# Kernel optimization log

Measured on AMD Instinct MI355X. Metric: run time of the kernel, lower is better.

The kernel has to match this reference:

```python
import jax, jax.numpy as jnp
import numpy as np

N, E = 100000, 1600000
IN_DIM, OUT_DIM, EDGE_DIM, HEADS = 128, 64, 16, 4
HEAD_DIM = OUT_DIM // HEADS


def setup_inputs() -> dict:
    key = jax.random.key(0)
    ks = jax.random.split(key, 8)
    x = jax.random.normal(ks[0], (N, IN_DIM), dtype=jnp.float32)
    ei = jax.random.randint(ks[1], (2, E), 0, N, dtype=jnp.int32)
    ea = jax.random.normal(ks[2], (E, EDGE_DIM), dtype=jnp.float32)
    # parameters (xavier-ish scaling)
    W_node = jax.random.normal(ks[3], (OUT_DIM, IN_DIM), dtype=jnp.float32) * (1.0 / np.sqrt(IN_DIM))
    W_edge = jax.random.normal(ks[4], (HEADS, EDGE_DIM), dtype=jnp.float32) * (1.0 / np.sqrt(EDGE_DIM))
    att_src = jax.random.normal(ks[5], (1, HEADS, HEAD_DIM), dtype=jnp.float32) * (1.0 / np.sqrt(HEAD_DIM))
    att_dst = jax.random.normal(ks[6], (1, HEADS, HEAD_DIM), dtype=jnp.float32) * (1.0 / np.sqrt(HEAD_DIM))
    bias = jnp.zeros((OUT_DIM,), dtype=jnp.float32)
    return {"x": x, "ei": ei, "ea": ea, "W_node": W_node, "W_edge": W_edge,
            "att_src": att_src, "att_dst": att_dst, "bias": bias}


def reference(x, ei, ea, W_node, W_edge, att_src, att_dst, bias):
    n = x.shape[0]
    Wh = (x @ W_node.T).reshape(n, HEADS, HEAD_DIM)          # [N,H,D]
    s, d = ei[0], ei[1]
    # per-node attention scalars, gathered per edge (avoids gathering Wh[d])
    a_src = jnp.sum(Wh * att_src, axis=-1)                    # [N,H]
    a_dst = jnp.sum(Wh * att_dst, axis=-1)                    # [N,H]
    e = jax.nn.leaky_relu(a_src[s] + a_dst[d] + ea @ W_edge.T, negative_slope=0.2)  # [E,H]
    ex = jnp.exp(e - jnp.max(e))                              # global max, as in torch e.max()
    den = jax.ops.segment_sum(ex, d, num_segments=n)          # [N,H]
    alpha = ex / (den[d] + 1e-9)                              # [E,H]
    msg = Wh[s] * alpha[:, :, None]                           # [E,H,D]
    out = jax.ops.segment_sum(msg, d, num_segments=n)         # [N,H,D]
    return jax.nn.elu(out.reshape(n, OUT_DIM) + bias)
```

## Files before the change

kernel.cpp:

```cpp
#include <hip/hip_runtime.h>
#include <math.h>

#define NN 100000
#define NE 1600000
#define IND 128
#define OUTD 64
#define ED 16
#define NH 4
#define HD 16
#define NB1 98

typedef float f4v __attribute__((ext_vector_type(4)));

__global__ __launch_bounds__(256) void k_node(
        const float* __restrict__ x, const float* __restrict__ Wn,
        const float* __restrict__ att_s, const float* __restrict__ att_d,
        float* __restrict__ Wh, float* __restrict__ asrc, float* __restrict__ adst,
        int* __restrict__ deg) {
    __shared__ float sWt[IND * OUTD];
    __shared__ float sx[16][IND];
    int tid = threadIdx.x;
    long long rowBase = (long long)blockIdx.x * 16;
    if (tid < 16 && rowBase + tid < NN) deg[rowBase + tid] = 0;
    {
        int c = tid & 63;
        for (int k4 = tid >> 6; k4 < IND / 4; k4 += 4) {
            float4 v = ((const float4*)Wn)[c * (IND / 4) + k4];
            sWt[(k4 * 4 + 0) * OUTD + c] = v.x;
            sWt[(k4 * 4 + 1) * OUTD + c] = v.y;
            sWt[(k4 * 4 + 2) * OUTD + c] = v.z;
            sWt[(k4 * 4 + 3) * OUTD + c] = v.w;
        }
    }
    for (int i = tid; i < 16 * (IND / 4); i += 256) {
        int r = i >> 5, k4 = i & 31;
        long long row = rowBase + r;
        float4 v = make_float4(0.f, 0.f, 0.f, 0.f);
        if (row < NN) v = ((const float4*)x)[row * (IND / 4) + k4];
        ((float4*)sx)[r * (IND / 4) + k4] = v;
    }
    __syncthreads();

    int wave = tid >> 6, lane = tid & 63;
    float acc0 = 0.f, acc1 = 0.f, acc2 = 0.f, acc3 = 0.f;
    const float4* xr0 = (const float4*)&sx[wave * 4 + 0][0];
    const float4* xr1 = (const float4*)&sx[wave * 4 + 1][0];
    const float4* xr2 = (const float4*)&sx[wave * 4 + 2][0];
    const float4* xr3 = (const float4*)&sx[wave * 4 + 3][0];
#pragma unroll 1
    for (int kk = 0; kk < IND / 16; kk++) {
#pragma unroll
        for (int j = 0; j < 4; j++) {
            int k4 = kk * 4 + j;
            float w0 = sWt[(k4 * 4 + 0) * OUTD + lane];
            float w1 = sWt[(k4 * 4 + 1) * OUTD + lane];
            float w2 = sWt[(k4 * 4 + 2) * OUTD + lane];
            float w3 = sWt[(k4 * 4 + 3) * OUTD + lane];
            float4 x0 = xr0[k4], x1 = xr1[k4], x2 = xr2[k4], x3 = xr3[k4];
            acc0 += x0.x * w0 + x0.y * w1 + x0.z * w2 + x0.w * w3;
            acc1 += x1.x * w0 + x1.y * w1 + x1.z * w2 + x1.w * w3;
            acc2 += x2.x * w0 + x2.y * w1 + x2.z * w2 + x2.w * w3;
            acc3 += x3.x * w0 + x3.y * w1 + x3.z * w2 + x3.w * w3;
        }
    }
    float as = att_s[lane];
    float ad = att_d[lane];
    float accs[4] = {acc0, acc1, acc2, acc3};
#pragma unroll
    for (int rr = 0; rr < 4; rr++) {
        long long row = rowBase + wave * 4 + rr;
        if (row >= NN) continue;
        Wh[row * OUTD + lane] = accs[rr];
        float vs = accs[rr] * as, vd = accs[rr] * ad;
#pragma unroll
        for (int m = 1; m < 16; m <<= 1) {
            vs += __shfl_xor(vs, m);
            vd += __shfl_xor(vd, m);
        }
        if ((lane & 15) == 0) {
            int h = lane >> 4;
            asrc[row * NH + h] = vs;
            adst[row * NH + h] = vd;
        }
    }
}

__global__ void k_hist(const int* __restrict__ ei, int* __restrict__ deg) {
    int i = blockIdx.x * 256 + threadIdx.x;
    if (i < NE / 4) {
        int4 dv = ((const int4*)(ei + NE))[i];
        atomicAdd(&deg[dv.x], 1);
        atomicAdd(&deg[dv.y], 1);
        atomicAdd(&deg[dv.z], 1);
        atomicAdd(&deg[dv.w], 1);
    }
}

__global__ __launch_bounds__(256) void k_scan1(const int* __restrict__ deg,
                                               int* __restrict__ offA,
                                               int* __restrict__ bsum) {
    __shared__ int sd[256];
    int b = blockIdx.x, t = threadIdx.x;
    int base = b * 1024 + t * 4;
    int v0 = 0, v1 = 0, v2 = 0, v3 = 0;
    if (base + 0 < NN) v0 = deg[base + 0];
    if (base + 1 < NN) v1 = deg[base + 1];
    if (base + 2 < NN) v2 = deg[base + 2];
    if (base + 3 < NN) v3 = deg[base + 3];
    int s = v0 + v1 + v2 + v3;
    sd[t] = s;
    __syncthreads();
    for (int ofs = 1; ofs < 256; ofs <<= 1) {
        int xv = 0;
        if (t >= ofs) xv = sd[t - ofs];
        __syncthreads();
        sd[t] += xv;
        __syncthreads();
    }
    int excl = sd[t] - s;
    if (base + 0 < NN) offA[base + 0] = excl;
    if (base + 1 < NN) offA[base + 1] = excl + v0;
    if (base + 2 < NN) offA[base + 2] = excl + v0 + v1;
    if (base + 3 < NN) offA[base + 3] = excl + v0 + v1 + v2;
    if (t == 255) bsum[b] = sd[255];
}

__global__ __launch_bounds__(128) void k_scan2(int* __restrict__ bsum) {
    __shared__ int sd[128];
    int t = threadIdx.x;
    int v = (t < NB1) ? bsum[t] : 0;
    sd[t] = v;
    __syncthreads();
    for (int ofs = 1; ofs < 128; ofs <<= 1) {
        int xv = 0;
        if (t >= ofs) xv = sd[t - ofs];
        __syncthreads();
        sd[t] += xv;
        __syncthreads();
    }
    if (t < NB1) bsum[t] = sd[t] - v;
}

__global__ void k_scan3(const int* __restrict__ offA, const int* __restrict__ bsum,
                        int* __restrict__ off, int* __restrict__ pos) {
    int i = blockIdx.x * 256 + threadIdx.x;
    if (i < NN) {
        int v = offA[i] + bsum[i >> 10];
        off[i] = v;
        pos[i] = v;
    }
    if (i == 0) off[NN] = NE;
}

__global__ __launch_bounds__(256) void k_edge(
        const int* __restrict__ ei, const float* __restrict__ ea,
        const float* __restrict__ We, const float* __restrict__ asrc,
        const float* __restrict__ adst, int* __restrict__ pos,
        float* __restrict__ rec) {
    __shared__ float sWe[NH * ED];
    if (threadIdx.x < NH * ED) sWe[threadIdx.x] = We[threadIdx.x];
    __syncthreads();
    int e = blockIdx.x * 256 + threadIdx.x;
    if (e >= NE) return;
    int s = ei[e];
    int d = ei[NE + e];
    int p = atomicAdd(&pos[d], 1);
    float4 as4 = *(const float4*)(asrc + (long long)s * NH);
    float4 ad4 = *(const float4*)(adst + (long long)d * NH);
    f4v* ea4 = (f4v*)(const_cast<float*>(ea) + (long long)e * ED);
    f4v q0 = __builtin_nontemporal_load(ea4 + 0);
    f4v q1 = __builtin_nontemporal_load(ea4 + 1);
    f4v q2 = __builtin_nontemporal_load(ea4 + 2);
    f4v q3 = __builtin_nontemporal_load(ea4 + 3);
    float asv[4] = {as4.x, as4.y, as4.z, as4.w};
    float adv[4] = {ad4.x, ad4.y, ad4.z, ad4.w};
    unsigned int u[4];
#pragma unroll
    for (int h = 0; h < NH; h++) {
        const float* w = sWe + h * ED;
        float t = asv[h] + adv[h];
        t += q0.x * w[0]  + q0.y * w[1]  + q0.z * w[2]  + q0.w * w[3];
        t += q1.x * w[4]  + q1.y * w[5]  + q1.z * w[6]  + q1.w * w[7];
        t += q2.x * w[8]  + q2.y * w[9]  + q2.z * w[10] + q2.w * w[11];
        t += q3.x * w[12] + q3.y * w[13] + q3.z * w[14] + q3.w * w[15];
        t = (t >= 0.f) ? t : 0.2f * t;
        u[h] = __float_as_uint(expf(t));
    }
    unsigned int ss = (unsigned int)s;
    u[0] = (u[0] & ~31u) | (ss & 31u);
    u[1] = (u[1] & ~15u) | ((ss >> 5) & 15u);
    u[2] = (u[2] & ~15u) | ((ss >> 9) & 15u);
    u[3] = (u[3] & ~15u) | ((ss >> 13) & 15u);
    f4v rv = {__uint_as_float(u[0]), __uint_as_float(u[1]),
              __uint_as_float(u[2]), __uint_as_float(u[3])};
    __builtin_nontemporal_store(rv, (f4v*)rec + p);
}

__global__ __launch_bounds__(256) void k_gather(
        const int* __restrict__ off, float* __restrict__ rec,
        const float* __restrict__ Wh, const float* __restrict__ bias,
        float* __restrict__ out) {
    int node = blockIdx.x * 4 + (threadIdx.x >> 6);
    int lane = threadIdx.x & 63;
    if (node >= NN) return;
    int start = off[node], end = off[node + 1];
    int g = lane >> 4;
    int c16 = lane & 15;
    int h = c16 >> 2;

    float accx = 0.f, accy = 0.f, accz = 0.f, accw = 0.f;
    float dsum = 0.f;
#pragma unroll 2
    for (int j = start + g; j < end; j += 4) {
        f4v r = __builtin_nontemporal_load((f4v*)rec + j);
        unsigned int b0 = __float_as_uint(r.x), b1 = __float_as_uint(r.y);
        unsigned int b2 = __float_as_uint(r.z), b3 = __float_as_uint(r.w);
        int src = (int)((b0 & 31u) | ((b1 & 15u) << 5) | ((b2 & 15u) << 9) | ((b3 & 15u) << 13));
        float ex = (h == 0) ? r.x : (h == 1) ? r.y : (h == 2) ? r.z : r.w;
        float4 w = *(const float4*)(Wh + (long long)src * OUTD + c16 * 4);
        accx += ex * w.x;
        accy += ex * w.y;
        accz += ex * w.z;
        accw += ex * w.w;
        dsum += ex;
    }
#pragma unroll
    for (int m = 16; m < 64; m <<= 1) {
        accx += __shfl_xor(accx, m);
        accy += __shfl_xor(accy, m);
        accz += __shfl_xor(accz, m);
        accw += __shfl_xor(accw, m);
        dsum += __shfl_xor(dsum, m);
    }
    if (g == 0) {
        float rden = 1.0f / (dsum + 1e-9f);
        const float4 b4 = *(const float4*)(bias + c16 * 4);
        float vx = accx * rden + b4.x;
        float vy = accy * rden + b4.y;
        float vz = accz * rden + b4.z;
        float vw = accw * rden + b4.w;
        vx = (vx > 0.f) ? vx : expm1f(vx);
        vy = (vy > 0.f) ? vy : expm1f(vy);
        vz = (vz > 0.f) ? vz : expm1f(vz);
        vw = (vw > 0.f) ? vw : expm1f(vw);
        f4v v = {vx, vy, vz, vw};
        __builtin_nontemporal_store(v, (f4v*)(out + (long long)node * OUTD) + c16);
    }
}

extern "C" void kernel_launch(void* const* d_in, const int* in_sizes, int n_in,
                              void* d_out, int out_size, void* d_ws, size_t ws_size,
                              hipStream_t stream) {
    const float* x     = (const float*)d_in[0];
    const int*   ei    = (const int*)d_in[1];
    const float* ea    = (const float*)d_in[2];
    const float* Wn    = (const float*)d_in[3];
    const float* We    = (const float*)d_in[4];
    const float* att_s = (const float*)d_in[5];
    const float* att_d = (const float*)d_in[6];
    const float* bias  = (const float*)d_in[7];
    float* out = (float*)d_out;

    float* ws   = (float*)d_ws;
    float* Wh   = ws;
    float* asrc = Wh + (size_t)NN * OUTD;
    float* adst = asrc + (size_t)NN * NH;
    float* rec  = adst + (size_t)NN * NH;
    int*   deg  = (int*)(rec + (size_t)NE * 4);
    int*   offA = deg + NN;
    int*   off  = offA + NN;
    int*   pos  = off + NN + 1;
    int*   bsum = pos + NN;

    k_node<<<(NN + 15) / 16, 256, 0, stream>>>(x, Wn, att_s, att_d, Wh, asrc, adst, deg);
    k_hist<<<(NE / 4 + 255) / 256, 256, 0, stream>>>(ei, deg);
    k_scan1<<<NB1, 256, 0, stream>>>(deg, offA, bsum);
    k_scan2<<<1, 128, 0, stream>>>(bsum);
    k_scan3<<<(NN + 255) / 256, 256, 0, stream>>>(offA, bsum, off, pos);
    k_edge<<<(NE + 255) / 256, 256, 0, stream>>>(ei, ea, We, asrc, adst, pos, rec);
    k_gather<<<(NN + 3) / 4, 256, 0, stream>>>(off, rec, Wh, bias, out);
}
```

Baseline: 482.9 us.

## Fuse degree histogram into node kernel and precompute per-edge rank

The degree histogram atomics move into the node-projection kernel, where each thread handles one edge (6250 blocks × 256 = 1.6M edges exactly) and keeps the atomic's return value as that edge's rank. The edge kernel then computes its CSR slot as off[d] + rank instead of doing a second atomicAdd on a position array. This removes one kernel launch and one full pass of 1.6M atomics, and lets the histogram atomics overlap with the GEMM's shared-memory loads. In exchange it adds a separate zeroing kernel and an extra 6.4 MB rank array write and read, and it depends on the grid sizes matching NE exactly, since the bounds checks were dropped.

```diff
diff --git a/kernel.cpp b/kernel.cpp
--- a/kernel.cpp
+++ b/kernel.cpp
@@ -12,16 +12,24 @@
 
 typedef float f4v __attribute__((ext_vector_type(4)));
 
+__global__ void k_zero(int* __restrict__ deg) {
+    int i = blockIdx.x * 256 + threadIdx.x;
+    if (i < NN) deg[i] = 0;
+}
+
 __global__ __launch_bounds__(256) void k_node(
         const float* __restrict__ x, const float* __restrict__ Wn,
         const float* __restrict__ att_s, const float* __restrict__ att_d,
         float* __restrict__ Wh, float* __restrict__ asrc, float* __restrict__ adst,
-        int* __restrict__ deg) {
+        const int* __restrict__ ei, int* __restrict__ deg, int* __restrict__ rnk) {
     __shared__ float sWt[IND * OUTD];
     __shared__ float sx[16][IND];
     int tid = threadIdx.x;
     long long rowBase = (long long)blockIdx.x * 16;
-    if (tid < 16 && rowBase + tid < NN) deg[rowBase + tid] = 0;
+
+    int e = blockIdx.x * 256 + tid;
+    int dd = ei[NE + e];
+
     {
         int c = tid & 63;
         for (int k4 = tid >> 6; k4 < IND / 4; k4 += 4) {
@@ -39,6 +47,9 @@
         if (row < NN) v = ((const float4*)x)[row * (IND / 4) + k4];
         ((float4*)sx)[r * (IND / 4) + k4] = v;
     }
+
+    rnk[e] = atomicAdd(&deg[dd], 1);
+
     __syncthreads();
 
     int wave = tid >> 6, lane = tid & 63;
@@ -82,17 +93,6 @@
             asrc[row * NH + h] = vs;
             adst[row * NH + h] = vd;
         }
-    }
-}
-
-__global__ void k_hist(const int* __restrict__ ei, int* __restrict__ deg) {
-    int i = blockIdx.x * 256 + threadIdx.x;
-    if (i < NE / 4) {
-        int4 dv = ((const int4*)(ei + NE))[i];
-        atomicAdd(&deg[dv.x], 1);
-        atomicAdd(&deg[dv.y], 1);
-        atomicAdd(&deg[dv.z], 1);
-        atomicAdd(&deg[dv.w], 1);
     }
 }
 
@@ -142,31 +142,27 @@
 }
 
 __global__ void k_scan3(const int* __restrict__ offA, const int* __restrict__ bsum,
-                        int* __restrict__ off, int* __restrict__ pos) {
+                        int* __restrict__ off) {
     int i = blockIdx.x * 256 + threadIdx.x;
-    if (i < NN) {
-        int v = offA[i] + bsum[i >> 10];
-        off[i] = v;
-        pos[i] = v;
-    }
+    if (i < NN) off[i] = offA[i] + bsum[i >> 10];
     if (i == 0) off[NN] = NE;
 }
 
 __global__ __launch_bounds__(256) void k_edge(
         const int* __restrict__ ei, const float* __restrict__ ea,
         const float* __restrict__ We, const float* __restrict__ asrc,
-        const float* __restrict__ adst, int* __restrict__ pos,
-        float* __restrict__ rec) {
+        const float* __restrict__ adst, const int* __restrict__ off,
+        const int* __restrict__ rnk, float* __restrict__ rec) {
     __shared__ float sWe[NH * ED];
     if (threadIdx.x < NH * ED) sWe[threadIdx.x] = We[threadIdx.x];
     __syncthreads();
     int e = blockIdx.x * 256 + threadIdx.x;
-    if (e >= NE) return;
     int s = ei[e];
     int d = ei[NE + e];
-    int p = atomicAdd(&pos[d], 1);
+    int r = rnk[e];
     float4 as4 = *(const float4*)(asrc + (long long)s * NH);
     float4 ad4 = *(const float4*)(adst + (long long)d * NH);
+    int p = off[d] + r;
     f4v* ea4 = (f4v*)(const_cast<float*>(ea) + (long long)e * ED);
     f4v q0 = __builtin_nontemporal_load(ea4 + 0);
     f4v q1 = __builtin_nontemporal_load(ea4 + 1);
@@ -269,14 +265,15 @@
     int*   deg  = (int*)(rec + (size_t)NE * 4);
     int*   offA = deg + NN;
     int*   off  = offA + NN;
-    int*   pos  = off + NN + 1;
-    int*   bsum = pos + NN;
-
-    k_node<<<(NN + 15) / 16, 256, 0, stream>>>(x, Wn, att_s, att_d, Wh, asrc, adst, deg);
-    k_hist<<<(NE / 4 + 255) / 256, 256, 0, stream>>>(ei, deg);
+    int*   bsum = off + NN + 1;
+    int*   rnk  = bsum + 128;
+
+    k_zero<<<(NN + 255) / 256, 256, 0, stream>>>(deg);
+    k_node<<<(NN + 15) / 16, 256, 0, stream>>>(x, Wn, att_s, att_d, Wh, asrc, adst,
+                                               ei, deg, rnk);
     k_scan1<<<NB1, 256, 0, stream>>>(deg, offA, bsum);
     k_scan2<<<1, 128, 0, stream>>>(bsum);
-    k_scan3<<<(NN + 255) / 256, 256, 0, stream>>>(offA, bsum, off, pos);
-    k_edge<<<(NE + 255) / 256, 256, 0, stream>>>(ei, ea, We, asrc, adst, pos, rec);
+    k_scan3<<<(NN + 255) / 256, 256, 0, stream>>>(offA, bsum, off);
+    k_edge<<<(NE + 255) / 256, 256, 0, stream>>>(ei, ea, We, asrc, adst, off, rnk, rec);
     k_gather<<<(NN + 3) / 4, 256, 0, stream>>>(off, rec, Wh, bias, out);
 }
```

New measurement: 428.9 us. 1.13x faster.
